# Kernel optimization log

Measured on AMD Instinct MI355X. Metric: run time of the kernel, lower is better.

Reference implementation:

```python
import jax, jax.numpy as jnp
import numpy as np

EPS = 1e-7
BETA = 50.0
THRESH = 5.0  # torch Softplus threshold applies to beta*x


def project(points, K, E, dist, H, W):
    # points (N,P,3); K (N,3,3) intrinsics; E (N,3,4) extrinsics; dist (N,2)
    N, P, _ = points.shape
    ph = jnp.concatenate([points, jnp.ones((N, P, 1), points.dtype)], axis=-1)  # (N,P,4)
    pi = jnp.einsum('nij,npj->nip', E, ph)  # (N,3,P) camera-space points
    z = pi[:, 2]
    z = jnp.where(jnp.abs(z) < EPS, 1.0, z)
    x = pi[:, 0] / z
    y = pi[:, 1] / z
    r2 = x * x + y * y
    f = 1.0 + dist[:, 0:1] * r2 + dist[:, 1:2] * r2 * r2  # radial distortion
    x = x * f
    y = y * f
    p = jnp.stack([x, y, jnp.ones_like(x)], axis=1)  # (N,3,P)
    pk = jnp.einsum('nij,njp->nip', K, p)
    u = 2.0 * pk[:, 0] / (W - 1.0) - 1.0
    v = 2.0 * pk[:, 1] / (H - 1.0) - 1.0
    return u, v


def grid_sample_zeros(img, u, v):
    # bilinear grid_sample, padding_mode='zeros', align_corners=False
    # img (N,C,H,W); u,v (N,P) normalized coords in [-1,1]; returns (N,C,P)
    N, C, H, W = img.shape
    x = (u + 1.0) * (W / 2.0) - 0.5
    y = (v + 1.0) * (H / 2.0) - 0.5
    x0 = jnp.floor(x)
    y0 = jnp.floor(y)
    wx = x - x0
    wy = y - y0
    x0i = x0.astype(jnp.int32)
    y0i = y0.astype(jnp.int32)
    imgf = img.reshape(N, C, H * W)

    def gather(ix, iy):
        valid = (ix >= 0) & (ix < W) & (iy >= 0) & (iy < H)
        idx = jnp.clip(iy, 0, H - 1) * W + jnp.clip(ix, 0, W - 1)
        vals = jnp.take_along_axis(imgf, idx[:, None, :], axis=2)  # (N,C,P)
        return vals * valid[:, None, :].astype(img.dtype)

    return (gather(x0i, y0i) * ((1 - wx) * (1 - wy))[:, None]
            + gather(x0i + 1, y0i) * (wx * (1 - wy))[:, None]
            + gather(x0i, y0i + 1) * ((1 - wx) * wy)[:, None]
            + gather(x0i + 1, y0i + 1) * (wx * wy)[:, None])


def softplus_b50(x):
    bx = BETA * x
    return jnp.where(bx > THRESH, x, jax.nn.softplus(bx) / BETA)


def setup_inputs() -> dict:
    key = jax.random.key(0)
    ks = jax.random.split(key, 8)
    B, V, F, H, W = 1, 8, 64, 256, 256
    G, GD = 128, 8
    return {
        'feature_maps': jax.random.normal(ks[0], (B, V, F, H, W), jnp.float32),
        'camera_intrinsics': jax.random.normal(ks[1], (B, V, 3, 3), jnp.float32),
        'camera_extrinsics': jax.random.normal(ks[2], (B, V, 3, 4), jnp.float32),
        'camera_distortions': jax.random.normal(ks[3], (B, V, 2), jnp.float32),
        'grids': jax.random.normal(ks[4], (B, G, 3, GD, GD, GD), jnp.float32),
        'visibilities': jax.random.uniform(ks[5], (B, V, G), jnp.float32),
        'normals': jax.random.normal(ks[6], (B, G, 3), jnp.float32),
        'camera_centers': jax.random.normal(ks[7], (B, V, 3), jnp.float32),
    }


def reference(feature_maps, camera_intrinsics, camera_extrinsics, camera_distortions,
              grids, visibilities, normals, camera_centers):
    B, V, F, H, W = feature_maps.shape
    _, G, _, GH, GW, GD = grids.shape
    S = GH * GW * GD
    # grids (B,G,3,GH,GW,GD) -> (B, G*S, 3), flatten order (G,GH,GW,GD)
    xyz = jnp.moveaxis(grids, 2, 5).reshape(B, G * S, 3)
    xyz_bv = jnp.broadcast_to(xyz[:, None], (B, V, G * S, 3)).reshape(B * V, G * S, 3)
    u, v = project(xyz_bv, camera_intrinsics.reshape(-1, 3, 3),
                   camera_extrinsics.reshape(-1, 3, 4),
                   camera_distortions.reshape(-1, 2), H, W)
    feat = grid_sample_zeros(feature_maps.reshape(B * V, F, H, W), u, v)  # (BV,F,G*S)
    feat = feat.reshape(B, V, F, G, GH, GW, GD).transpose(0, 1, 3, 2, 4, 5, 6)  # (B,V,G,F,GH,GW,GD)
    inside = ((u >= -1.0) & (u <= 1.0) & (v >= -1.0) & (v <= 1.0))
    inside = inside.reshape(B, V, G, GH, GW, GD).astype(feature_maps.dtype)
    # view directions and cos angle with surface normals
    dirs = xyz[:, None] - camera_centers[:, :, None]  # (B,V,G*S,3)
    dirs = dirs / jnp.clip(jnp.linalg.norm(dirs, axis=-1, keepdims=True), 1e-12)
    dirs = dirs.reshape(B, V, G, S, 3)
    cos = jnp.einsum('bvgsc,bgc->bvgs', dirs, normals)
    cos = jnp.minimum(cos, 0.0).reshape(B, V, G, GH, GW, GD)
    w = visibilities[:, :, :, None, None, None] * (-cos) * inside
    w = softplus_b50(w)
    w = w / jnp.sum(w, axis=1, keepdims=True)
    w = w[:, :, :, None]  # (B,V,G,1,GH,GW,GD)
    wmean = jnp.sum(feat * w, axis=1)
    wvar = jnp.sum(feat * feat * w, axis=1) - wmean * wmean
    return jnp.concatenate([wmean, wvar], axis=2)  # (B,G,2F,GH,GW,GD)
```

## Files before the change

kernel.cpp:

```cpp
#include <hip/hip_runtime.h>
#include <hip/hip_fp16.h>
#include <math.h>

#define VFS_EPS 1e-7f

constexpr int V_ = 8, F_ = 64, H_ = 256, W_ = 256, G_ = 128, S_ = 512;
constexpr int HW_ = H_ * W_;
constexpr int TPX = 512;

__global__ __launch_bounds__(512) void vfs_transpose_h(const float* __restrict__ src,
                                                       __half* __restrict__ dst) {
    __shared__ ushort L[TPX][64];
    const int v = blockIdx.y;
    const int p0 = blockIdx.x * TPX;
    const int t = threadIdx.x;
    const float* s = src + (size_t)v * F_ * HW_ + p0;
#pragma unroll 8
    for (int c = 0; c < F_; ++c) {
        const float val = s[(size_t)c * HW_ + t];
        const int os = (c >> 3) ^ (t & 7);
        L[t][os * 8 + (c & 7)] = __half_as_ushort(__float2half(val));
    }
    __syncthreads();
    __half* d = dst + ((size_t)v * HW_ + p0) * F_;
#pragma unroll
    for (int i = 0; i < 8; ++i) {
        const int j = i * 512 + t;
        const int p = j >> 3;
        const int o = j & 7;
        const int os = o ^ (p & 7);
        const uint4 val = *reinterpret_cast<const uint4*>(&L[p][os * 8]);
        *reinterpret_cast<uint4*>(&d[(size_t)j * 8]) = val;
    }
}

__global__ __launch_bounds__(256) void vfs_sampler_h2(
    const __half* __restrict__ feat,
    const float* __restrict__ Km, const float* __restrict__ Em,
    const float* __restrict__ dst, const float* __restrict__ grids,
    const float* __restrict__ vis, const float* __restrict__ normals,
    const float* __restrict__ cc, float* __restrict__ out) {
    __shared__ float4 wp[64][8];
    __shared__ float wv[64][8];
    __shared__ float stgM[64][65];
    __shared__ float stgV[64][65];

    const int g = blockIdx.x >> 3;
    const int sb = (blockIdx.x & 7) * 64;
    const int t = threadIdx.x;
    const int wave = t >> 6;
    const int lane = t & 63;

    {
        const int vL = lane & 7;
        const int pL = lane >> 3;
        const float nx = normals[g * 3 + 0];
        const float ny = normals[g * 3 + 1];
        const float nz = normals[g * 3 + 2];
#pragma unroll
        for (int grp = 0; grp < 2; ++grp) {
            const int sl = wave * 16 + grp * 8 + pL;
            const int s = sb + sl;
            const float px = grids[(g * 3 + 0) * S_ + s];
            const float py = grids[(g * 3 + 1) * S_ + s];
            const float pz = grids[(g * 3 + 2) * S_ + s];
            const float* Ev = Em + vL * 12;
            const float pi0 = Ev[0] * px + Ev[1] * py + Ev[2] * pz + Ev[3];
            const float pi1 = Ev[4] * px + Ev[5] * py + Ev[6] * pz + Ev[7];
            float z = Ev[8] * px + Ev[9] * py + Ev[10] * pz + Ev[11];
            if (fabsf(z) < VFS_EPS) z = 1.0f;
            const float xn = pi0 / z;
            const float yn = pi1 / z;
            const float r2 = xn * xn + yn * yn;
            const float fd = 1.0f + dst[vL * 2 + 0] * r2 + dst[vL * 2 + 1] * r2 * r2;
            const float xd = xn * fd, yd = yn * fd;
            const float* Kv = Km + vL * 9;
            const float pk0 = Kv[0] * xd + Kv[1] * yd + Kv[2];
            const float pk1 = Kv[3] * xd + Kv[4] * yd + Kv[5];
            const float u = 2.0f * pk0 / (W_ - 1.0f) - 1.0f;
            const float vq = 2.0f * pk1 / (H_ - 1.0f) - 1.0f;
            const bool inside = (u >= -1.0f) && (u <= 1.0f) && (vq >= -1.0f) && (vq <= 1.0f);
            const float x = (u + 1.0f) * (W_ * 0.5f) - 0.5f;
            const float y = (vq + 1.0f) * (H_ * 0.5f) - 0.5f;
            const float x0f = floorf(x), y0f = floorf(y);
            const float wx = x - x0f, wy = y - y0f;
            const int x0 = (int)x0f, y0 = (int)y0f;
            const float dx = px - cc[vL * 3 + 0];
            const float dy = py - cc[vL * 3 + 1];
            const float dz = pz - cc[vL * 3 + 2];
            float nrm = sqrtf(dx * dx + dy * dy + dz * dz);
            nrm = fmaxf(nrm, 1e-12f);
            float cosv = (dx * nx + dy * ny + dz * nz) / nrm;
            cosv = fminf(cosv, 0.0f);
            const float wraw = vis[vL * G_ + g] * (-cosv) * (inside ? 1.0f : 0.0f);
            const float bx = 50.0f * wraw;
            float w = (bx > 5.0f) ? wraw : (log1pf(expf(bx)) * (1.0f / 50.0f));
            float wsum = w;
            wsum += __shfl_xor(wsum, 1);
            wsum += __shfl_xor(wsum, 2);
            wsum += __shfl_xor(wsum, 4);
            w = w / wsum;
            wp[sl][vL] = make_float4(__int_as_float(x0), __int_as_float(y0), wx, wy);
            wv[sl][vL] = w;
        }
    }
    __syncthreads();

    const int sub = lane >> 5;
    const int cp = lane & 31;
    const uint* fp = reinterpret_cast<const uint*>(feat);
    for (int jj = 0; jj < 8; ++jj) {
        const int sl = wave * 16 + jj * 2 + sub;
        float mx = 0.f, my = 0.f, qx = 0.f, qy = 0.f;
#pragma unroll
        for (int v = 0; v < 8; ++v) {
            const float4 q = wp[sl][v];
            const float w = wv[sl][v];
            const int x0 = __float_as_int(q.x);
            const int y0 = __float_as_int(q.y);
            const float wx = q.z, wy = q.w;
            const bool vx0 = (x0 >= 0) & (x0 < W_);
            const bool vx1 = (x0 >= -1) & (x0 < W_ - 1);
            const bool vy0 = (y0 >= 0) & (y0 < H_);
            const bool vy1 = (y0 >= -1) & (y0 < H_ - 1);
            const int xc0 = min(max(x0, 0), W_ - 1);
            const int xc1 = min(max(x0 + 1, 0), W_ - 1);
            const int yc0 = min(max(y0, 0), H_ - 1);
            const int yc1 = min(max(y0 + 1, 0), H_ - 1);
            const uint base = (uint)(v * HW_) * 32u + (uint)cp;
            const uint i00 = base + (uint)(yc0 * W_ + xc0) * 32u;
            const uint i01 = base + (uint)(yc0 * W_ + xc1) * 32u;
            const uint i10 = base + (uint)(yc1 * W_ + xc0) * 32u;
            const uint i11 = base + (uint)(yc1 * W_ + xc1) * 32u;
            const float2 g00 = __half22float2(*reinterpret_cast<const __half2*>(fp + i00));
            const float2 g01 = __half22float2(*reinterpret_cast<const __half2*>(fp + i01));
            const float2 g10 = __half22float2(*reinterpret_cast<const __half2*>(fp + i10));
            const float2 g11 = __half22float2(*reinterpret_cast<const __half2*>(fp + i11));
            const float f00 = (vx0 & vy0) ? (1.f - wx) * (1.f - wy) : 0.f;
            const float f01 = (vx1 & vy0) ? wx * (1.f - wy) : 0.f;
            const float f10 = (vx0 & vy1) ? (1.f - wx) * wy : 0.f;
            const float f11 = (vx1 & vy1) ? wx * wy : 0.f;
            const float fex = g00.x * f00 + g01.x * f01 + g10.x * f10 + g11.x * f11;
            const float fey = g00.y * f00 + g01.y * f01 + g10.y * f10 + g11.y * f11;
            mx += w * fex;
            qx += w * fex * fex;
            my += w * fey;
            qy += w * fey * fey;
        }
        stgM[sl][2 * cp + 0] = mx;
        stgM[sl][2 * cp + 1] = my;
        stgV[sl][2 * cp + 0] = qx - mx * mx;
        stgV[sl][2 * cp + 1] = qy - my * my;
    }
    __syncthreads();

#pragma unroll
    for (int i = 0; i < 16; ++i) {
        const int e = t + i * 256;
        const int f = e >> 6;
        const int sl = e & 63;
        out[((size_t)(g * 2 * F_ + f)) * S_ + sb + sl] = stgM[sl][f];
    }
#pragma unroll
    for (int i = 0; i < 16; ++i) {
        const int e = t + i * 256;
        const int f = e >> 6;
        const int sl = e & 63;
        out[((size_t)(g * 2 * F_ + F_ + f)) * S_ + sb + sl] = stgV[sl][f];
    }
}

__global__ __launch_bounds__(256) void vfs_sampler_f32(
    const float* __restrict__ feat,
    const float* __restrict__ Km, const float* __restrict__ Em,
    const float* __restrict__ dst, const float* __restrict__ grids,
    const float* __restrict__ vis, const float* __restrict__ normals,
    const float* __restrict__ cc, float* __restrict__ out) {
    __shared__ float4 wp[64][8];
    __shared__ float wv[64][8];
    __shared__ float stg[64][65];

    const int g = blockIdx.x >> 3;
    const int sb = (blockIdx.x & 7) * 64;
    const int t = threadIdx.x;
    const int wave = t >> 6;
    const int lane = t & 63;
    const int vL = lane & 7;
    const int pL = lane >> 3;

    const float nx = normals[g * 3 + 0];
    const float ny = normals[g * 3 + 1];
    const float nz = normals[g * 3 + 2];

#pragma unroll
    for (int grp = 0; grp < 2; ++grp) {
        const int sl = wave * 16 + grp * 8 + pL;
        const int s = sb + sl;
        const float px = grids[(g * 3 + 0) * S_ + s];
        const float py = grids[(g * 3 + 1) * S_ + s];
        const float pz = grids[(g * 3 + 2) * S_ + s];
        const float* Ev = Em + vL * 12;
        const float pi0 = Ev[0] * px + Ev[1] * py + Ev[2] * pz + Ev[3];
        const float pi1 = Ev[4] * px + Ev[5] * py + Ev[6] * pz + Ev[7];
        float z = Ev[8] * px + Ev[9] * py + Ev[10] * pz + Ev[11];
        if (fabsf(z) < VFS_EPS) z = 1.0f;
        const float xn = pi0 / z;
        const float yn = pi1 / z;
        const float r2 = xn * xn + yn * yn;
        const float fd = 1.0f + dst[vL * 2 + 0] * r2 + dst[vL * 2 + 1] * r2 * r2;
        const float xd = xn * fd, yd = yn * fd;
        const float* Kv = Km + vL * 9;
        const float pk0 = Kv[0] * xd + Kv[1] * yd + Kv[2];
        const float pk1 = Kv[3] * xd + Kv[4] * yd + Kv[5];
        const float u = 2.0f * pk0 / (W_ - 1.0f) - 1.0f;
        const float vq = 2.0f * pk1 / (H_ - 1.0f) - 1.0f;
        const bool inside = (u >= -1.0f) && (u <= 1.0f) && (vq >= -1.0f) && (vq <= 1.0f);
        const float x = (u + 1.0f) * (W_ * 0.5f) - 0.5f;
        const float y = (vq + 1.0f) * (H_ * 0.5f) - 0.5f;
        const float x0f = floorf(x), y0f = floorf(y);
        const float wx = x - x0f, wy = y - y0f;
        const int x0 = (int)x0f, y0 = (int)y0f;
        const float dx = px - cc[vL * 3 + 0];
        const float dy = py - cc[vL * 3 + 1];
        const float dz = pz - cc[vL * 3 + 2];
        float nrm = sqrtf(dx * dx + dy * dy + dz * dz);
        nrm = fmaxf(nrm, 1e-12f);
        float cosv = (dx * nx + dy * ny + dz * nz) / nrm;
        cosv = fminf(cosv, 0.0f);
        const float wraw = vis[vL * G_ + g] * (-cosv) * (inside ? 1.0f : 0.0f);
        const float bx = 50.0f * wraw;
        float w = (bx > 5.0f) ? wraw : (log1pf(expf(bx)) * (1.0f / 50.0f));
        float wsum = w;
        wsum += __shfl_xor(wsum, 1);
        wsum += __shfl_xor(wsum, 2);
        wsum += __shfl_xor(wsum, 4);
        w = w / wsum;
        wp[sl][vL] = make_float4(__int_as_float(x0), __int_as_float(y0), wx, wy);
        wv[sl][vL] = w;
    }
    __syncthreads();

    float mean[16], var[16];
#pragma unroll 2
    for (int j = 0; j < 16; ++j) {
        const int sl = wave * 16 + j;
        float m = 0.0f, m2 = 0.0f;
#pragma unroll
        for (int v = 0; v < 8; ++v) {
            const float4 q = wp[sl][v];
            const float w = wv[sl][v];
            const int x0 = __float_as_int(q.x);
            const int y0 = __float_as_int(q.y);
            const float wx = q.z, wy = q.w;
            const bool vx0 = (x0 >= 0) & (x0 < W_);
            const bool vx1 = (x0 >= -1) & (x0 < W_ - 1);
            const bool vy0 = (y0 >= 0) & (y0 < H_);
            const bool vy1 = (y0 >= -1) & (y0 < H_ - 1);
            const int xc0 = min(max(x0, 0), W_ - 1);
            const int xc1 = min(max(x0 + 1, 0), W_ - 1);
            const int yc0 = min(max(y0, 0), H_ - 1);
            const int yc1 = min(max(y0 + 1, 0), H_ - 1);
            const float* base = feat + (size_t)v * ((size_t)HW_ * F_) + (size_t)lane * HW_;
            const float g00 = base[(size_t)(yc0 * W_ + xc0)];
            const float g01 = base[(size_t)(yc0 * W_ + xc1)];
            const float g10 = base[(size_t)(yc1 * W_ + xc0)];
            const float g11 = base[(size_t)(yc1 * W_ + xc1)];
            const float f00 = (vx0 & vy0) ? (1.f - wx) * (1.f - wy) : 0.f;
            const float f01 = (vx1 & vy0) ? wx * (1.f - wy) : 0.f;
            const float f10 = (vx0 & vy1) ? (1.f - wx) * wy : 0.f;
            const float f11 = (vx1 & vy1) ? wx * wy : 0.f;
            const float fe = g00 * f00 + g01 * f01 + g10 * f10 + g11 * f11;
            m += w * fe;
            m2 += w * fe * fe;
        }
        mean[j] = m;
        var[j] = m2 - m * m;
    }

#pragma unroll
    for (int j = 0; j < 16; ++j) stg[wave * 16 + j][lane] = mean[j];
    __syncthreads();
#pragma unroll
    for (int i = 0; i < 16; ++i) {
        const int e = t + i * 256;
        const int f = e >> 6;
        const int sl = e & 63;
        out[((size_t)(g * 2 * F_ + f)) * S_ + sb + sl] = stg[sl][f];
    }
    __syncthreads();
#pragma unroll
    for (int j = 0; j < 16; ++j) stg[wave * 16 + j][lane] = var[j];
    __syncthreads();
#pragma unroll
    for (int i = 0; i < 16; ++i) {
        const int e = t + i * 256;
        const int f = e >> 6;
        const int sl = e & 63;
        out[((size_t)(g * 2 * F_ + F_ + f)) * S_ + sb + sl] = stg[sl][f];
    }
}

extern "C" void kernel_launch(void* const* d_in, const int* in_sizes, int n_in,
                              void* d_out, int out_size, void* d_ws, size_t ws_size,
                              hipStream_t stream) {
    const float* fm      = (const float*)d_in[0];
    const float* Km      = (const float*)d_in[1];
    const float* Em      = (const float*)d_in[2];
    const float* dist    = (const float*)d_in[3];
    const float* grids   = (const float*)d_in[4];
    const float* vis     = (const float*)d_in[5];
    const float* normals = (const float*)d_in[6];
    const float* cc      = (const float*)d_in[7];
    float* out           = (float*)d_out;

    const size_t tsize = (size_t)V_ * F_ * HW_ * sizeof(__half);
    if (ws_size >= tsize) {
        vfs_transpose_h<<<dim3(HW_ / TPX, V_), 512, 0, stream>>>(fm, (__half*)d_ws);
        vfs_sampler_h2<<<G_ * 8, 256, 0, stream>>>((const __half*)d_ws, Km, Em, dist,
                                                   grids, vis, normals, cc, out);
    } else {
        vfs_sampler_f32<<<G_ * 8, 256, 0, stream>>>(fm, Km, Em, dist,
                                                    grids, vis, normals, cc, out);
    }
}
```

Before: 76.71 us.

## Gather adjacent x-pixels with one wave-wide load and share across half-waves

Each wave now handles one sample at a time instead of two. Each of the two 32-lane halves loads one of the two horizontally adjacent pixels (64 contiguous halves per row), so every tap needs only two row loads, and the 2x2 neighbourhood is rebuilt with a cross-half shuffle. All loads for the 8 views are issued up front, and the per-sample coordinates are made wave-uniform with readfirstlane. In exchange the FMA work per lane doubles, since both halves compute the same result and each writes only mean or only variance, and the shuffles plus register-held loads add overhead.

```diff
diff --git a/kernel.cpp b/kernel.cpp
--- a/kernel.cpp
+++ b/kernel.cpp
@@ -7,6 +7,12 @@
 constexpr int V_ = 8, F_ = 64, H_ = 256, W_ = 256, G_ = 128, S_ = 512;
 constexpr int HW_ = H_ * W_;
 constexpr int TPX = 512;
+
+__device__ __forceinline__ __half2 vfs_uint_as_half2(uint u) {
+    union { uint u; __half2 h; } c;
+    c.u = u;
+    return c.h;
+}
 
 __global__ __launch_bounds__(512) void vfs_transpose_h(const float* __restrict__ src,
                                                        __half* __restrict__ dst) {
@@ -106,40 +112,53 @@
     }
     __syncthreads();
 
-    const int sub = lane >> 5;
+    const int hs = lane >> 5;
     const int cp = lane & 31;
     const uint* fp = reinterpret_cast<const uint*>(feat);
-    for (int jj = 0; jj < 8; ++jj) {
-        const int sl = wave * 16 + jj * 2 + sub;
+
+    for (int j = 0; j < 16; ++j) {
+        const int sl = wave * 16 + j;
+        uint u0[8], u1[8];
+#pragma unroll
+        for (int v = 0; v < 8; ++v) {
+            const float4 q = wp[sl][v];
+            const int x0 = __builtin_amdgcn_readfirstlane(__float_as_int(q.x));
+            const int y0 = __builtin_amdgcn_readfirstlane(__float_as_int(q.y));
+            const int xs = min(max(x0, 0), W_ - 2);
+            const int yc0 = min(max(y0, 0), H_ - 1);
+            const int yc1 = min(max(y0 + 1, 0), H_ - 1);
+            u0[v] = fp[((uint)(v * HW_ + yc0 * W_ + xs) << 5) + (uint)lane];
+            u1[v] = fp[((uint)(v * HW_ + yc1 * W_ + xs) << 5) + (uint)lane];
+        }
         float mx = 0.f, my = 0.f, qx = 0.f, qy = 0.f;
 #pragma unroll
         for (int v = 0; v < 8; ++v) {
             const float4 q = wp[sl][v];
             const float w = wv[sl][v];
-            const int x0 = __float_as_int(q.x);
-            const int y0 = __float_as_int(q.y);
+            const int x0 = __builtin_amdgcn_readfirstlane(__float_as_int(q.x));
+            const int y0 = __builtin_amdgcn_readfirstlane(__float_as_int(q.y));
             const float wx = q.z, wy = q.w;
+            const int xs = min(max(x0, 0), W_ - 2);
+            const int p0 = min(max(x0, 0), W_ - 1) - xs;
+            const int p1 = min(max(x0 + 1, 0), W_ - 1) - xs;
+            const uint o0 = (uint)__shfl_xor((int)u0[v], 32);
+            const uint o1 = (uint)__shfl_xor((int)u1[v], 32);
+            const uint c00 = (p0 == hs) ? u0[v] : o0;
+            const uint c01 = (p1 == hs) ? u0[v] : o0;
+            const uint c10 = (p0 == hs) ? u1[v] : o1;
+            const uint c11 = (p1 == hs) ? u1[v] : o1;
             const bool vx0 = (x0 >= 0) & (x0 < W_);
             const bool vx1 = (x0 >= -1) & (x0 < W_ - 1);
             const bool vy0 = (y0 >= 0) & (y0 < H_);
             const bool vy1 = (y0 >= -1) & (y0 < H_ - 1);
-            const int xc0 = min(max(x0, 0), W_ - 1);
-            const int xc1 = min(max(x0 + 1, 0), W_ - 1);
-            const int yc0 = min(max(y0, 0), H_ - 1);
-            const int yc1 = min(max(y0 + 1, 0), H_ - 1);
-            const uint base = (uint)(v * HW_) * 32u + (uint)cp;
-            const uint i00 = base + (uint)(yc0 * W_ + xc0) * 32u;
-            const uint i01 = base + (uint)(yc0 * W_ + xc1) * 32u;
-            const uint i10 = base + (uint)(yc1 * W_ + xc0) * 32u;
-            const uint i11 = base + (uint)(yc1 * W_ + xc1) * 32u;
-            const float2 g00 = __half22float2(*reinterpret_cast<const __half2*>(fp + i00));
-            const float2 g01 = __half22float2(*reinterpret_cast<const __half2*>(fp + i01));
-            const float2 g10 = __half22float2(*reinterpret_cast<const __half2*>(fp + i10));
-            const float2 g11 = __half22float2(*reinterpret_cast<const __half2*>(fp + i11));
             const float f00 = (vx0 & vy0) ? (1.f - wx) * (1.f - wy) : 0.f;
             const float f01 = (vx1 & vy0) ? wx * (1.f - wy) : 0.f;
             const float f10 = (vx0 & vy1) ? (1.f - wx) * wy : 0.f;
             const float f11 = (vx1 & vy1) ? wx * wy : 0.f;
+            const float2 g00 = __half22float2(vfs_uint_as_half2(c00));
+            const float2 g01 = __half22float2(vfs_uint_as_half2(c01));
+            const float2 g10 = __half22float2(vfs_uint_as_half2(c10));
+            const float2 g11 = __half22float2(vfs_uint_as_half2(c11));
             const float fex = g00.x * f00 + g01.x * f01 + g10.x * f10 + g11.x * f11;
             const float fey = g00.y * f00 + g01.y * f01 + g10.y * f10 + g11.y * f11;
             mx += w * fex;
@@ -147,10 +166,13 @@
             my += w * fey;
             qy += w * fey * fey;
         }
-        stgM[sl][2 * cp + 0] = mx;
-        stgM[sl][2 * cp + 1] = my;
-        stgV[sl][2 * cp + 0] = qx - mx * mx;
-        stgV[sl][2 * cp + 1] = qy - my * my;
+        if (hs == 0) {
+            stgM[sl][2 * cp + 0] = mx;
+            stgM[sl][2 * cp + 1] = my;
+        } else {
+            stgV[sl][2 * cp + 0] = qx - mx * mx;
+            stgV[sl][2 * cp + 1] = qy - my * my;
+        }
     }
     __syncthreads();
 
```

Result: slower. 95.97 us (+25.1%).
